# Optimization experiments

Measured on AMD Instinct MI355X. Metric: run time of the kernel, lower is better.

## Reference

```python
import jax, jax.numpy as jnp
import numpy as np
import math

B, N, DIN, H, DH, DV, DENC, MAXLEN = 8, 1024, 1024, 8, 128, 64, 32, 1024
EPS = 1e-5


def _make_pe():
    # sinusoidal table, stored as a learnable parameter in the torch module
    pos = np.arange(MAXLEN, dtype=np.float32)[:, None]
    div = np.exp(np.arange(0, DENC, 2, dtype=np.float32) * (-math.log(10000.0) / DENC))
    pe = np.zeros((MAXLEN, DENC), np.float32)
    pe[:, 0::2] = np.sin(pos * div)
    pe[:, 1::2] = np.cos(pos * div)
    return jnp.asarray(pe)[None]  # (1, MAXLEN, DENC)


def setup_inputs() -> dict:
    key = jax.random.key(0)
    ks = jax.random.split(key, 4)
    dq = DH * H  # = d_q = d_k = 1024
    return {
        "x": jax.random.normal(ks[0], (B, N, DIN), jnp.float32),
        "gamma": jnp.ones((1, 1, DIN), jnp.float32),
        "beta": jnp.zeros((1, 1, DIN), jnp.float32),
        "pe": _make_pe(),
        "W_pos": jax.random.normal(ks[1], (DIN + DENC, DIN), jnp.float32) * 0.02,
        "b_pos": jnp.zeros((DIN,), jnp.float32),
        "W_qkv": jax.random.normal(ks[2], (DIN, 2 * dq + DV * H), jnp.float32) * 0.02,
        "b_qkv": jnp.zeros((2 * dq + DV * H,), jnp.float32),
        "W_out": jax.random.normal(ks[3], (DV * H, DIN), jnp.float32) * 0.02,
        "b_out": jnp.zeros((DIN,), jnp.float32),
        "scale": jnp.asarray(1.414, jnp.float32),
    }


def reference(x, gamma, beta, pe, W_pos, b_pos, W_qkv, b_qkv, W_out, b_out, scale):
    Bq, Nq, _ = x.shape
    # PositionalEncoding: concat sinusoidal table, project back to d_in, residual add
    pos_in = jnp.concatenate([x, jnp.broadcast_to(pe[:, :Nq], (Bq, Nq, DENC))], axis=-1)
    h = x + (pos_in @ W_pos + b_pos)
    # FeatureNorm: normalize over the SEQUENCE dim (dim=1), biased variance
    mean = h.mean(axis=1, keepdims=True)
    var = h.var(axis=1, keepdims=True)
    hn = gamma * (h - mean) * jax.lax.rsqrt(var + EPS) + beta
    # QKV projection and head split
    qkv = hn @ W_qkv + b_qkv
    dq = DH * H
    q = qkv[..., :dq].reshape(Bq, Nq, H, DH).transpose(0, 2, 1, 3)       # (B,H,N,DH)
    k = qkv[..., dq:2 * dq].reshape(Bq, Nq, H, DH).transpose(0, 2, 1, 3)  # (B,H,N,DH)
    v = qkv[..., 2 * dq:].reshape(Bq, Nq, H, DV).transpose(0, 2, 1, 3)    # (B,H,N,DV)
    # for_twdit branch: attn = softmax(-(cdist(q,k)/scale)^2) == softmax(-||q-k||^2/scale^2)
    sq = jnp.sum(q * q, axis=-1)  # (B,H,N)
    sk = jnp.sum(k * k, axis=-1)  # (B,H,N)
    d2 = sq[..., :, None] + sk[..., None, :] - 2.0 * jnp.einsum('bhnc,bhmc->bhnm', q, k)
    d2 = jnp.maximum(d2, 0.0)  # cdist is a true (nonnegative) distance
    attn = jax.nn.softmax(-d2 / (scale * scale), axis=-1)  # (B,H,N,N)
    out = jnp.einsum('bhnm,bhmd->bhnd', attn, v)            # (B,H,N,DV)
    out = out.transpose(0, 2, 1, 3).reshape(Bq, Nq, H * DV)
    return x + (out @ W_out + b_out)
```

## Files before the change

### kernel.cpp

```cpp
#include <hip/hip_runtime.h>
#include <math.h>

typedef __bf16 bf16;
typedef __attribute__((ext_vector_type(8))) __bf16 bf16x8;
typedef __attribute__((ext_vector_type(4))) float f32x4;

#define MFMA16(a, b, c) __builtin_amdgcn_mfma_f32_16x16x32_bf16(a, b, c, 0, 0, 0)

__device__ __forceinline__ void gld_lds16(const void* g, void* l) {
  __builtin_amdgcn_global_load_lds(
      (const __attribute__((address_space(1))) unsigned int*)g,
      (__attribute__((address_space(3))) unsigned int*)l, 16, 0, 0);
}

__global__ __launch_bounds__(256) void prep_kernel(
    const float* __restrict__ x, const float* __restrict__ W_pos,
    const float* __restrict__ W_qkv, const float* __restrict__ W_out,
    const float* __restrict__ pe,
    bf16* __restrict__ x_bf, bf16* __restrict__ wpos_p, bf16* __restrict__ wqkv_p,
    bf16* __restrict__ wout_p, bf16* __restrict__ pe_pj) {
  __shared__ float tile[32][33];
  const int tid = threadIdx.x;
  int blk = blockIdx.x;
  if (blk < 4096) {
    int idx = blk * 256 + tid;
    const float4 a = ((const float4*)x)[idx * 2];
    const float4 b = ((const float4*)x)[idx * 2 + 1];
    bf16x8 o = {(bf16)a.x, (bf16)a.y, (bf16)a.z, (bf16)a.w,
                (bf16)b.x, (bf16)b.y, (bf16)b.z, (bf16)b.w};
    *(bf16x8*)(x_bf + (size_t)idx * 8) = o;
    return;
  }
  blk -= 4096;
  if (blk < 4096) {
    const float* W; bf16* BP; int K, N, bx, by;
    if (blk < 1024)      { W = W_pos; BP = wpos_p; K = 1024; N = 1024; bx = blk & 31; by = blk >> 5; }
    else if (blk < 3584) { int b2 = blk - 1024; W = W_qkv; BP = wqkv_p; K = 1024; N = 2560; bx = b2 % 80; by = b2 / 80; }
    else                 { int b2 = blk - 3584; W = W_out; BP = wout_p; K = 512;  N = 1024; bx = b2 & 31; by = b2 >> 5; }
    const int n0 = bx * 32, k0 = by * 32;
    const int tx = tid & 31, ty = tid >> 5;
#pragma unroll
    for (int i = 0; i < 4; ++i)
      tile[ty + 8 * i][tx] = W[(size_t)(k0 + ty + 8 * i) * N + n0 + tx];
    __syncthreads();
    if (tid < 128) {
      int cc = tid & 31, kq = tid >> 5;
      int c = n0 + cc, k = k0 + kq * 8;
      bf16x8 v;
#pragma unroll
      for (int i = 0; i < 8; ++i) v[i] = (bf16)tile[kq * 8 + i][cc];
      *(bf16x8*)(BP + ((size_t)(c >> 4) * (K >> 3) + (k >> 3)) * 128 + (c & 15) * 8) = v;
    }
    return;
  }
  blk -= 4096;
  int idx = blk * 256 + tid;
  int n = idx >> 10, c = idx & 1023;
  float s = 0.f;
#pragma unroll
  for (int e = 0; e < 32; ++e)
    s += pe[n * 32 + e] * W_pos[(size_t)(1024 + e) * 1024 + c];
  pe_pj[idx] = (bf16)s;
}

template <int NT, int OUT_BF16>
__global__ __launch_bounds__(256, 3) void gemm_bd(
    const bf16* __restrict__ A, const bf16* __restrict__ BP, void* __restrict__ Cout,
    int M, int N, int K,
    const float* __restrict__ bias, const bf16* __restrict__ add_full,
    const bf16* __restrict__ add_mod) {
  __shared__ __align__(16) bf16 As[3][128 * 64];
  const int tid = threadIdx.x;
  const int wave = tid >> 6, lane = tid & 63;
  const int wr = wave >> 1, wc = wave & 1;
  const int lr = lane & 15, lg = lane >> 4;
  const int KB = K >> 3;

  const int nwg = gridDim.x * gridDim.y;
  const int bid = blockIdx.y * gridDim.x + blockIdx.x;
  const int s = (bid & 7) * (nwg >> 3) + (bid >> 3);
  const int row0 = (s / gridDim.x) * 128, col0 = (s % gridDim.x) * 128;
  const int cb0 = (col0 >> 4) + wc * 4;

  const int trow = tid >> 3;
  const int cbd = ((tid & 7) * 16) ^ ((trow & 7) << 4);
  const bf16* asrc = A + (size_t)(row0 + trow) * K + (cbd >> 1);
  f32x4 acc[4][4] = {};

  auto STAGE = [&](int sel, int t) {
    char* al = (char*)&As[sel][0] + tid * 16;
#pragma unroll
    for (int c = 0; c < 4; ++c)
      gld_lds16(asrc + (size_t)c * 32 * K + t * 64, al + c * 4096);
  };

  STAGE(0, 0);
  STAGE(1, 1);
  asm volatile("s_waitcnt vmcnt(4)" ::: "memory");
  __builtin_amdgcn_s_barrier();

#pragma unroll
  for (int t = 0; t < NT; ++t) {
    if (t + 2 < NT) STAGE((t + 2) % 3, t + 2);
    const char* Ab = (const char*)&As[t % 3][0];
#pragma unroll
    for (int kc = 0; kc < 2; ++kc) {
      const int kb = (t << 3) + kc * 4 + lg;
      bf16x8 bfr[4], af[4];
#pragma unroll
      for (int nt = 0; nt < 4; ++nt)
        bfr[nt] = *(const bf16x8*)(BP + ((size_t)(cb0 + nt) * KB + kb) * 128 + lr * 8);
#pragma unroll
      for (int mt = 0; mt < 4; ++mt) {
        int r = wr * 64 + mt * 16 + lr;
        af[mt] = *(const bf16x8*)(Ab + r * 128 + ((kc * 64 + lg * 16) ^ ((r & 7) << 4)));
      }
      __builtin_amdgcn_s_setprio(1);
#pragma unroll
      for (int mt = 0; mt < 4; ++mt)
#pragma unroll
        for (int nt = 0; nt < 4; ++nt)
          acc[mt][nt] = MFMA16(af[mt], bfr[nt], acc[mt][nt]);
      __builtin_amdgcn_s_setprio(0);
    }
    if (t + 2 < NT)
      asm volatile("s_waitcnt vmcnt(4)" ::: "memory");
    else
      asm volatile("s_waitcnt vmcnt(0)" ::: "memory");
    __builtin_amdgcn_s_barrier();
  }

#pragma unroll
  for (int mt = 0; mt < 4; ++mt) {
#pragma unroll
    for (int v = 0; v < 4; ++v) {
      int r = row0 + wr * 64 + mt * 16 + lg * 4 + v;
#pragma unroll
      for (int nt = 0; nt < 4; ++nt) {
        int c = col0 + wc * 64 + nt * 16 + lr;
        float val = acc[mt][nt][v];
        if (bias) val += bias[c];
        if (add_full) val += (float)add_full[(size_t)r * N + c];
        if (add_mod) val += (float)add_mod[(size_t)(r & 1023) * N + c];
        if (OUT_BF16)
          ((bf16*)Cout)[(size_t)r * N + c] = (bf16)val;
        else
          ((float*)Cout)[(size_t)r * N + c] = val;
      }
    }
  }
}

__global__ __launch_bounds__(512) void featnorm_kernel(const bf16* __restrict__ h,
                                                       bf16* __restrict__ hn,
                                                       const float* __restrict__ gamma,
                                                       const float* __restrict__ beta) {
  const int b = blockIdx.x >> 4;
  const int d0 = (blockIdx.x & 15) << 6;
  const int tid = threadIdx.x;
  const int c = tid & 63, g = tid >> 6;
  const size_t base = (size_t)b * (1024 * 1024) + d0 + c;
  float s = 0.f, s2 = 0.f;
  for (int n = g * 128; n < g * 128 + 128; ++n) {
    float v = (float)h[base + (size_t)n * 1024];
    s += v; s2 += v * v;
  }
  __shared__ float rs[8][64], rs2[8][64];
  rs[g][c] = s; rs2[g][c] = s2;
  __syncthreads();
  __shared__ float smean[64], srstd[64];
  if (tid < 64) {
    float S = 0.f, S2 = 0.f;
#pragma unroll
    for (int q = 0; q < 8; ++q) { S += rs[q][tid]; S2 += rs2[q][tid]; }
    float mean = S * (1.f / 1024.f);
    float var = S2 * (1.f / 1024.f) - mean * mean;
    smean[tid] = mean;
    srstd[tid] = rsqrtf(var + 1e-5f);
  }
  __syncthreads();
  const float mean = smean[c], rstd = srstd[c];
  const float gm = gamma[d0 + c], bt = beta[d0 + c];
  for (int n = g * 128; n < g * 128 + 128; ++n) {
    size_t idx = base + (size_t)n * 1024;
    hn[idx] = (bf16)(gm * ((float)h[idx] - mean) * rstd + bt);
  }
}

__global__ __launch_bounds__(256) void skvt_kernel(const bf16* __restrict__ qkv,
                                                   const float* __restrict__ scale_ptr,
                                                   float* __restrict__ skl,
                                                   bf16* __restrict__ vT) {
  const int tid = threadIdx.x;
  if (blockIdx.x < 4096) {
    const int lr = tid & 15;
    const int task = blockIdx.x * 16 + (tid >> 4);
    const int bh = task >> 10, n = task & 1023;
    const int b = bh >> 3, h = bh & 7;
    const bf16x8 v = *(const bf16x8*)(qkv + (size_t)(b * 1024 + n) * 2560 +
                                      1024 + h * 128 + lr * 8);
    float s = 0.f;
#pragma unroll
    for (int i = 0; i < 8; ++i) { float f = (float)v[i]; s += f * f; }
#pragma unroll
    for (int off = 1; off < 16; off <<= 1) s += __shfl_xor(s, off);
    if (lr == 0) {
      float sc = scale_ptr[0];
      skl[task] = s * (1.44269504f / (sc * sc));
    }
    return;
  }
  __shared__ bf16 tile[32][34];
  const int blk = blockIdx.x - 4096;
  const int b = blk >> 9;
  const int rem = blk & 511;
  const int c0 = (rem >> 5) * 32, n0 = (rem & 31) * 32;
  const int tx = tid & 31, ty = tid >> 5;
#pragma unroll
  for (int i = 0; i < 4; ++i)
    tile[ty + 8 * i][tx] = qkv[(size_t)(b * 1024 + n0 + ty + 8 * i) * 2560 + 2048 + c0 + tx];
  __syncthreads();
#pragma unroll
  for (int i = 0; i < 4; ++i)
    vT[(size_t)(b * 512 + c0 + ty + 8 * i) * 1024 + n0 + tx] = tile[tx][ty + 8 * i];
}

__global__ __launch_bounds__(512, 4) void attn_mfma(const bf16* __restrict__ qkv,
                                                    const bf16* __restrict__ vT,
                                                    const float* __restrict__ skl,
                                                    const float* __restrict__ scale_ptr,
                                                    bf16* __restrict__ attn_o) {
  const int swz = ((blockIdx.x & 7) << 6) + (blockIdx.x >> 3);
  const int it = swz & 7, bh = swz >> 3;
  const int b = bh >> 3, h = bh & 7;
  const int i0 = it * 128;
  const int tid = threadIdx.x, wave = tid >> 6, lane = tid & 63;
  const int lr = lane & 15, lg = lane >> 4;
  const float sc = scale_ptr[0];
  const float c2 = 2.f * 1.44269504f / (sc * sc);

  __shared__ __align__(16) bf16 Ks[2][64 * 128];
  __shared__ __align__(16) bf16 Vs[2][64 * 64];
  __shared__ __align__(16) bf16 Ps[8][16 * 64];
  __shared__ float sks[1024];

  const int trowK = tid >> 4;
  const int cbKd = ((tid & 15) * 16) ^ ((trowK & 7) << 4);
  const bf16* ksrc = qkv + (size_t)(b * 1024 + trowK) * 2560 + 1024 + h * 128 + (cbKd >> 1);
  const int trowV = tid >> 3;
  const int cbVd = ((tid & 7) * 16) ^ ((trowV & 7) << 4);
  const bf16* vsrc = vT + (size_t)(b * 512 + h * 64 + trowV) * 1024 + (cbVd >> 1);

  auto STAGE = [&](int sel, int jt) {
    const bf16* kp = ksrc + (size_t)jt * 64 * 2560;
    char* kl = (char*)&Ks[sel][0] + tid * 16;
    gld_lds16(kp, kl);
    gld_lds16(kp + (size_t)32 * 2560, kl + 8192);
    gld_lds16(vsrc + jt * 64, (char*)&Vs[sel][0] + tid * 16);
  };

  {
    float2 sv = ((const float2*)(skl + (size_t)bh * 1024))[tid];
    *(float2*)&sks[tid * 2] = sv;
  }
  bf16x8 qf[4];
  {
    const bf16* qrow = qkv + (size_t)(b * 1024 + i0 + wave * 16 + lr) * 2560 + h * 128;
#pragma unroll
    for (int kc = 0; kc < 4; ++kc) qf[kc] = *(const bf16x8*)(qrow + kc * 32 + lg * 8);
  }
  __syncthreads();

  bf16x8 vones;
  {
    bf16 one_or_zero = (lr == 0) ? (bf16)1.0f : (bf16)0.0f;
#pragma unroll
    for (int i = 0; i < 8; ++i) vones[i] = one_or_zero;
  }

  f32x4 o[4] = {};
  f32x4 o_l = {};

  STAGE(0, 0);
  asm volatile("s_waitcnt vmcnt(0)" ::: "memory");
  __builtin_amdgcn_s_barrier();

#pragma unroll
  for (int jt = 0; jt < 16; ++jt) {
    const int cur = jt & 1;
    if (jt < 15) STAGE(cur ^ 1, jt + 1);

    f32x4 sacc[4] = {};
    __builtin_amdgcn_s_setprio(1);
#pragma unroll
    for (int kc = 0; kc < 4; ++kc) {
#pragma unroll
      for (int nt = 0; nt < 4; ++nt) {
        int j = nt * 16 + lr;
        int byte = j * 256 + (((kc * 32 + lg * 8) * 2) ^ ((j & 7) << 4));
        bf16x8 kf = *(const bf16x8*)((const char*)&Ks[cur][0] + byte);
        sacc[nt] = MFMA16(qf[kc], kf, sacc[nt]);
      }
    }
    __builtin_amdgcn_s_setprio(0);

#pragma unroll
    for (int nt = 0; nt < 4; ++nt) {
      float skv = sks[jt * 64 + nt * 16 + lr];
#pragma unroll
      for (int v = 0; v < 4; ++v) {
        float p = __builtin_amdgcn_exp2f(sacc[nt][v] * c2 - skv);
        int r = lg * 4 + v, c = nt * 16 + lr;
        int byte = r * 128 + ((c * 2) ^ ((r & 7) << 4));
        *(bf16*)((char*)&Ps[wave][0] + byte) = (bf16)p;
      }
    }
    bf16x8 pf[2];
#pragma unroll
    for (int kc = 0; kc < 2; ++kc) {
      int byte = lr * 128 + (((kc * 32 + lg * 8) * 2) ^ ((lr & 7) << 4));
      pf[kc] = *(const bf16x8*)((const char*)&Ps[wave][0] + byte);
    }
    __builtin_amdgcn_s_setprio(1);
#pragma unroll
    for (int kc = 0; kc < 2; ++kc) {
#pragma unroll
      for (int nt = 0; nt < 4; ++nt) {
        int d = nt * 16 + lr;
        int byte = d * 128 + (((kc * 32 + lg * 8) * 2) ^ ((d & 7) << 4));
        bf16x8 vf = *(const bf16x8*)((const char*)&Vs[cur][0] + byte);
        o[nt] = MFMA16(pf[kc], vf, o[nt]);
      }
      o_l = MFMA16(pf[kc], vones, o_l);
    }
    __builtin_amdgcn_s_setprio(0);

    asm volatile("s_waitcnt vmcnt(0)" ::: "memory");
    __builtin_amdgcn_s_barrier();
  }

#pragma unroll
  for (int v = 0; v < 4; ++v) {
    float ls = __shfl(o_l[v], lg << 4);
    float inv = 1.f / ls;
    int r = i0 + wave * 16 + lg * 4 + v;
#pragma unroll
    for (int nt = 0; nt < 4; ++nt) {
      int c = h * 64 + nt * 16 + lr;
      attn_o[(size_t)(b * 1024 + r) * 512 + c] = (bf16)(o[nt][v] * inv);
    }
  }
}

extern "C" void kernel_launch(void* const* d_in, const int* in_sizes, int n_in,
                              void* d_out, int out_size, void* d_ws, size_t ws_size,
                              hipStream_t stream) {
  const float* x     = (const float*)d_in[0];
  const float* gamma = (const float*)d_in[1];
  const float* beta  = (const float*)d_in[2];
  const float* pe    = (const float*)d_in[3];
  const float* W_pos = (const float*)d_in[4];
  const float* b_pos = (const float*)d_in[5];
  const float* W_qkv = (const float*)d_in[6];
  const float* b_qkv = (const float*)d_in[7];
  const float* W_out = (const float*)d_in[8];
  const float* b_out = (const float*)d_in[9];
  const float* scale = (const float*)d_in[10];
  float* outp = (float*)d_out;

  char* ws = (char*)d_ws;
  const size_t MB = 1 << 20;
  bf16* x_bf   = (bf16*)(ws);
  bf16* wpos_p = (bf16*)(ws + 16 * MB);
  bf16* wqkv_p = (bf16*)(ws + 18 * MB);
  bf16* wout_p = (bf16*)(ws + 23 * MB);
  bf16* pe_pj  = (bf16*)(ws + 24 * MB);
  bf16* vT     = (bf16*)(ws + 24 * MB);
  bf16* h      = (bf16*)(ws + 32 * MB);
  bf16* attn_o = (bf16*)(ws + 32 * MB);
  bf16* qkv    = (bf16*)(ws + 48 * MB);
  float* skl   = (float*)(ws + 88 * MB);
  bf16* hn     = (bf16*)(ws + 96 * MB);

  prep_kernel<<<12288, 256, 0, stream>>>(x, W_pos, W_qkv, W_out, pe,
                                         x_bf, wpos_p, wqkv_p, wout_p, pe_pj);
  gemm_bd<16, 1><<<dim3(8, 64), 256, 0, stream>>>(x_bf, wpos_p, h, 8192, 1024, 1024,
                                                  b_pos, x_bf, pe_pj);
  featnorm_kernel<<<128, 512, 0, stream>>>(h, hn, gamma, beta);
  gemm_bd<16, 1><<<dim3(20, 64), 256, 0, stream>>>(hn, wqkv_p, qkv, 8192, 2560, 1024,
                                                   b_qkv, nullptr, nullptr);
  skvt_kernel<<<8192, 256, 0, stream>>>(qkv, scale, skl, vT);
  attn_mfma<<<512, 512, 0, stream>>>(qkv, vT, skl, scale, attn_o);
  gemm_bd<8, 0><<<dim3(8, 64), 256, 0, stream>>>(attn_o, wout_p, outp, 8192, 1024, 512,
                                                 b_out, x_bf, nullptr);
}
```

Measured before the change: 243.6 us.

## Write normalized activations in MFMA fragment layout and add LDS-free QKV GEMM

The feature-norm kernel now writes its output in a pre-packed 16-row by 8-column block layout that matches the MFMA operand fragments. Its stores are vectorized 8-wide along the feature dimension. A new GEMM kernel for the QKV projection reads A and B fragments straight from global memory into registers, with no LDS staging, and adds the bias in the epilogue. This aims to drop the shared-memory traffic and barrier cost of the tiled GEMM. The trade-off is reliance on L2/cache reuse for operands shared across waves, and the kernel hardcodes 32 k-iterations (K=1024).

```diff
diff --git a/kernel.cpp b/kernel.cpp
--- a/kernel.cpp
+++ b/kernel.cpp
@@ -151,8 +151,59 @@
   }
 }
 
+__global__ __launch_bounds__(256, 4) void gemm_ff(
+    const bf16* __restrict__ AP, const bf16* __restrict__ BP, bf16* __restrict__ Cout,
+    int M, int N, int K, const float* __restrict__ bias) {
+  const int tid = threadIdx.x;
+  const int wave = tid >> 6, lane = tid & 63;
+  const int wr = wave >> 1, wc = wave & 1;
+  const int lr = lane & 15, lg = lane >> 4;
+  const int KB = K >> 3;
+
+  const int nwg = gridDim.x * gridDim.y;
+  const int bid = blockIdx.y * gridDim.x + blockIdx.x;
+  const int s = (bid & 7) * (nwg >> 3) + (bid >> 3);
+  const int row0 = (s / gridDim.x) * 128, col0 = (s % gridDim.x) * 128;
+  const int rb0 = (row0 >> 4) + wr * 4;
+  const int cb0 = (col0 >> 4) + wc * 4;
+
+  const bf16* ap = AP + (size_t)rb0 * KB * 128 + lr * 8;
+  const bf16* bp = BP + (size_t)cb0 * KB * 128 + lr * 8;
+  f32x4 acc[4][4] = {};
+
+#pragma unroll 4
+  for (int kk = 0; kk < 32; ++kk) {
+    const int kb = kk * 4 + lg;
+    bf16x8 af[4], bfr[4];
+#pragma unroll
+    for (int mt = 0; mt < 4; ++mt)
+      af[mt] = *(const bf16x8*)(ap + ((size_t)mt * KB + kb) * 128);
+#pragma unroll
+    for (int nt = 0; nt < 4; ++nt)
+      bfr[nt] = *(const bf16x8*)(bp + ((size_t)nt * KB + kb) * 128);
+#pragma unroll
+    for (int mt = 0; mt < 4; ++mt)
+#pragma unroll
+      for (int nt = 0; nt < 4; ++nt)
+        acc[mt][nt] = MFMA16(af[mt], bfr[nt], acc[mt][nt]);
+  }
+
+#pragma unroll
+  for (int mt = 0; mt < 4; ++mt) {
+#pragma unroll
+    for (int v = 0; v < 4; ++v) {
+      int r = row0 + wr * 64 + mt * 16 + lg * 4 + v;
+#pragma unroll
+      for (int nt = 0; nt < 4; ++nt) {
+        int c = col0 + wc * 64 + nt * 16 + lr;
+        Cout[(size_t)r * N + c] = (bf16)(acc[mt][nt][v] + bias[c]);
+      }
+    }
+  }
+}
+
 __global__ __launch_bounds__(512) void featnorm_kernel(const bf16* __restrict__ h,
-                                                       bf16* __restrict__ hn,
+                                                       bf16* __restrict__ hnp,
                                                        const float* __restrict__ gamma,
                                                        const float* __restrict__ beta) {
   const int b = blockIdx.x >> 4;
@@ -179,11 +230,24 @@
     srstd[tid] = rsqrtf(var + 1e-5f);
   }
   __syncthreads();
-  const float mean = smean[c], rstd = srstd[c];
-  const float gm = gamma[d0 + c], bt = beta[d0 + c];
-  for (int n = g * 128; n < g * 128 + 128; ++n) {
-    size_t idx = base + (size_t)n * 1024;
-    hn[idx] = (bf16)(gm * ((float)h[idx] - mean) * rstd + bt);
+
+  const int oct = tid & 7, slot = tid >> 3;
+  float mean8[8], rstd8[8], gm8[8], bt8[8];
+#pragma unroll
+  for (int j = 0; j < 8; ++j) {
+    int dl = oct * 8 + j;
+    mean8[j] = smean[dl]; rstd8[j] = srstd[dl];
+    gm8[j] = gamma[d0 + dl]; bt8[j] = beta[d0 + dl];
+  }
+  for (int it = 0; it < 16; ++it) {
+    int n = it * 64 + slot;
+    size_t r = (size_t)b * 1024 + n;
+    bf16x8 hv = *(const bf16x8*)(h + r * 1024 + d0 + oct * 8);
+    bf16x8 ov;
+#pragma unroll
+    for (int j = 0; j < 8; ++j)
+      ov[j] = (bf16)(gm8[j] * ((float)hv[j] - mean8[j]) * rstd8[j] + bt8[j]);
+    *(bf16x8*)(hnp + ((r >> 4) * 128 + (d0 >> 3) + oct) * 128 + (r & 15) * 8) = ov;
   }
 }
 
@@ -380,15 +444,14 @@
   bf16* attn_o = (bf16*)(ws + 32 * MB);
   bf16* qkv    = (bf16*)(ws + 48 * MB);
   float* skl   = (float*)(ws + 88 * MB);
-  bf16* hn     = (bf16*)(ws + 96 * MB);
+  bf16* hnp    = (bf16*)(ws + 96 * MB);
 
   prep_kernel<<<12288, 256, 0, stream>>>(x, W_pos, W_qkv, W_out, pe,
                                          x_bf, wpos_p, wqkv_p, wout_p, pe_pj);
   gemm_bd<16, 1><<<dim3(8, 64), 256, 0, stream>>>(x_bf, wpos_p, h, 8192, 1024, 1024,
                                                   b_pos, x_bf, pe_pj);
-  featnorm_kernel<<<128, 512, 0, stream>>>(h, hn, gamma, beta);
-  gemm_bd<16, 1><<<dim3(20, 64), 256, 0, stream>>>(hn, wqkv_p, qkv, 8192, 2560, 1024,
-                                                   b_qkv, nullptr, nullptr);
+  featnorm_kernel<<<128, 512, 0, stream>>>(h, hnp, gamma, beta);
+  gemm_ff<<<dim3(20, 64), 256, 0, stream>>>(hnp, wqkv_p, qkv, 8192, 2560, 1024, b_qkv);
   skvt_kernel<<<8192, 256, 0, stream>>>(qkv, scale, skl, vT);
   attn_mfma<<<512, 512, 0, stream>>>(qkv, vT, skl, scale, attn_o);
   gemm_bd<8, 0><<<dim3(8, 64), 256, 0, stream>>>(attn_o, wout_p, outp, 8192, 1024, 512,
```

After: 263.1 us. +8.0%, slower.
